# Kernel optimization log

Hardware: AMD Instinct MI355X
Metric: run time of the kernel (lower is better)

Reference implementation:

```python
import jax, jax.numpy as jnp
import numpy as np

B, S, D = 8, 512, 512
IN_S = IN_D = IN_E = 32
OUT_S = OUT_D = OUT_E = 32


def setup_inputs() -> dict:
    key = jax.random.key(0)
    ks = jax.random.split(key, 16)
    sc = 0.1
    return {
        "x_s": jax.random.normal(ks[0], (B, S, IN_S), jnp.float32),
        "x_d": jax.random.normal(ks[1], (B, D, IN_D), jnp.float32),
        "x_e": jax.random.normal(ks[2], (B, S, D, IN_E), jnp.float32),
        "W_ss": jax.random.normal(ks[3], (OUT_S, IN_S), jnp.float32) * sc,
        "b_ss": jnp.zeros((OUT_S,), jnp.float32),
        "W_se": jax.random.normal(ks[4], (OUT_S, IN_E), jnp.float32) * sc,
        "a_se_w": jax.random.normal(ks[5], (IN_E,), jnp.float32) * sc,
        "a_se_b": jnp.zeros((), jnp.float32),
        "W_dd": jax.random.normal(ks[6], (OUT_D, IN_D), jnp.float32) * sc,
        "b_dd": jnp.zeros((OUT_D,), jnp.float32),
        "W_de": jax.random.normal(ks[7], (OUT_D, IN_E), jnp.float32) * sc,
        "a_de_w": jax.random.normal(ks[8], (IN_E,), jnp.float32) * sc,
        "a_de_b": jnp.zeros((), jnp.float32),
        "W_ee": jax.random.normal(ks[9], (OUT_E, IN_E), jnp.float32) * sc,
        "b_ee": jnp.zeros((OUT_E,), jnp.float32),
        "W_es": jax.random.normal(ks[10], (OUT_E, IN_S), jnp.float32) * sc,
        "W_ed": jax.random.normal(ks[11], (OUT_E, IN_D), jnp.float32) * sc,
    }


def reference(x_s, x_d, x_e, W_ss, b_ss, W_se, a_se_w, a_se_b,
              W_dd, b_dd, W_de, a_de_w, a_de_b, W_ee, b_ee, W_es, W_ed):
    # Supply update: attention softmax over demand axis (dim=2)
    att_s = jax.nn.softmax(jnp.einsum('bsde,e->bsd', x_e, a_se_w) + a_se_b, axis=2)
    proj_se = jnp.einsum('bsde,oe->bsdo', x_e, W_se)
    h_s = jnp.einsum('bsi,oi->bso', x_s, W_ss) + b_ss \
        + jnp.einsum('bsdo,bsd->bso', proj_se, att_s)

    # Demand update: attention softmax over supply axis (dim=1)
    att_d = jax.nn.softmax(jnp.einsum('bsde,e->bsd', x_e, a_de_w) + a_de_b, axis=1)
    proj_de = jnp.einsum('bsde,oe->bsdo', x_e, W_de)
    h_d = jnp.einsum('bdi,oi->bdo', x_d, W_dd) + b_dd \
        + jnp.einsum('bsdo,bsd->bdo', proj_de, att_d)

    # Edge update: edge linear + broadcast node projections
    h_e = jnp.einsum('bsde,oe->bsdo', x_e, W_ee) + b_ee \
        + jnp.einsum('bsi,oi->bso', x_s, W_es)[:, :, None, :] \
        + jnp.einsum('bdi,oi->bdo', x_d, W_ed)[:, None, :, :]
    return (h_s, h_d, h_e)
```

## Files before the change

kernel.cpp:

```cpp
#include <hip/hip_runtime.h>
#include <cstddef>

#define B_ 8
#define S_ 512
#define D_ 512
#define TS 8
#define NST 64
#define DH 256

#define WS_BASES 0
#define WS_PES   131072
#define WS_BASED 262144
#define WS_PED   393216
#define WS_UD    524288
#define WS_ZD    (WS_UD + B_*NST*D_*32)
#define WS_US    (WS_ZD + B_*NST*D_)
#define WS_ZS    (WS_US + B_*S_*2*32)

#define HS_OFF 0
#define HD_OFF 131072
#define HE_OFF 262144

__global__ __launch_bounds__(256)
void k0_nodes(const float* __restrict__ x_s, const float* __restrict__ x_d,
              const float* __restrict__ W_ss, const float* __restrict__ b_ss,
              const float* __restrict__ W_dd, const float* __restrict__ b_dd,
              const float* __restrict__ W_es, const float* __restrict__ W_ed,
              float* __restrict__ ws)
{
  int g = blockIdx.x * 256 + threadIdx.x;
  int row = g >> 5, o = g & 31;
  bool sup = row < (B_ * S_);
  int r = sup ? row : row - B_ * S_;
  const float* x  = (sup ? x_s : x_d) + r * 32;
  const float* W1 = sup ? W_ss : W_dd;
  const float* W2 = sup ? W_es : W_ed;
  const float* bb = sup ? b_ss : b_dd;
  float xr[32];
#pragma unroll
  for (int k = 0; k < 8; k++)
    *(float4*)&xr[4*k] = *(const float4*)(x + 4*k);
  float acc1 = bb[o], acc2 = 0.f;
#pragma unroll
  for (int e = 0; e < 32; e++) {
    acc1 += xr[e] * W1[o*32 + e];
    acc2 += xr[e] * W2[o*32 + e];
  }
  int ob = sup ? WS_BASES : WS_BASED;
  int op = sup ? WS_PES  : WS_PED;
  ws[ob + r*32 + o] = acc1;
  ws[op + r*32 + o] = acc2;
}

__global__ __launch_bounds__(256, 3)
void k1_main(const float* __restrict__ x_e,
             const float* __restrict__ a_se_w, const float* __restrict__ a_se_b,
             const float* __restrict__ a_de_w, const float* __restrict__ a_de_b,
             const float* __restrict__ W_ee, const float* __restrict__ b_ee,
             float* __restrict__ ws,
             float* __restrict__ out)
{
  __shared__ float lds_ud[DH * 33];
  __shared__ float lds_hb[TS * 32];

  const int t = threadIdx.x;
  const int s_idx = t >> 5, d_off = t & 31;
  const int st = blockIdx.x, b = blockIdx.y, z = blockIdx.z;
  const int s = st * TS + s_idx;
  const int d0 = z * DH;

  for (int idx = t; idx < DH * 33; idx += 256) lds_ud[idx] = 0.f;
  lds_hb[t] = ws[WS_PES + (b*S_ + st*TS + (t>>5))*32 + (t&31)] + b_ee[t&31];
  __syncthreads();

  const float* xrow  = x_e + ((size_t)(b * S_ + s) * D_ + d0) * 32;
  float*       herow = out + HE_OFF + ((size_t)(b * S_ + s) * D_ + d0) * 32;
  const float* peD   = ws + WS_PED + ((size_t)b * D_ + d0) * 32;

  float us_acc[32];
#pragma unroll
  for (int e = 0; e < 32; e++) us_acc[e] = 0.f;
  float zs_acc = 0.f;
  const float asb = a_se_b[0], adb = a_de_b[0];

  float4 xb[8];
#pragma unroll
  for (int k = 0; k < 8; k++)
    xb[k] = *(const float4*)(xrow + d_off*32 + 4*k);

#pragma unroll 1
  for (int i = 0; i < 8; i++) {
    const int d = i*32 + d_off;
    float x[32];
#pragma unroll
    for (int k = 0; k < 8; k++) {
      x[4*k+0] = xb[k].x; x[4*k+1] = xb[k].y;
      x[4*k+2] = xb[k].z; x[4*k+3] = xb[k].w;
    }
    const int dn = (i < 7) ? d + 32 : d;
#pragma unroll
    for (int k = 0; k < 8; k++)
      xb[k] = *(const float4*)(xrow + dn*32 + 4*k);

    float ls = asb, ldt = adb;
#pragma unroll
    for (int e = 0; e < 32; e++) {
      ls  += x[e] * a_se_w[e];
      ldt += x[e] * a_de_w[e];
    }
    float es = __expf(ls), ed = __expf(ldt);
    zs_acc += es;
#pragma unroll
    for (int e = 0; e < 32; e++) us_acc[e] += es * x[e];

#pragma unroll
    for (int oq = 0; oq < 8; oq++) {
      float4 pdq = *(const float4*)(peD + d*32 + 4*oq);
      float4 hb  = *(const float4*)&lds_hb[s_idx*32 + 4*oq];
      float a0 = 0.f, a1 = 0.f, a2 = 0.f, a3 = 0.f;
#pragma unroll
      for (int e = 0; e < 32; e++) {
        a0 += x[e] * W_ee[(4*oq+0)*32 + e];
        a1 += x[e] * W_ee[(4*oq+1)*32 + e];
        a2 += x[e] * W_ee[(4*oq+2)*32 + e];
        a3 += x[e] * W_ee[(4*oq+3)*32 + e];
      }
      float4 r;
      r.x = a0 + hb.x + pdq.x;
      r.y = a1 + hb.y + pdq.y;
      r.z = a2 + hb.z + pdq.z;
      r.w = a3 + hb.w + pdq.w;
      *(float4*)(herow + d*32 + 4*oq) = r;
    }

#pragma unroll
    for (int e = 0; e < 32; e++)
      atomicAdd(&lds_ud[d*33 + e], ed * x[e]);
    atomicAdd(&lds_ud[d*33 + 32], ed);
  }
  __syncthreads();

  float* wud = ws + WS_UD + ((size_t)(b * NST + st) * D_ + d0) * 32;
  float* wzd = ws + WS_ZD + (b * NST + st) * D_ + d0;
#pragma unroll 1
  for (int sw = 0; sw < 8; sw++) {
    int r = sw * 32 + (t >> 3), g = t & 7;
    *(float4*)(wud + r*32 + g*4) = *(float4*)&lds_ud[r*33 + g*4];
  }
  wzd[t] = lds_ud[t*33 + 32];
  __syncthreads();

  float* red = lds_ud;
#pragma unroll
  for (int k = 0; k < 8; k++) {
    float4 v;
    v.x = us_acc[4*k+0]; v.y = us_acc[4*k+1];
    v.z = us_acc[4*k+2]; v.w = us_acc[4*k+3];
    *(float4*)&red[t*33 + 4*k] = v;
  }
  red[t*33 + 32] = zs_acc;
  __syncthreads();

  float sum = 0.f, zsum = 0.f;
#pragma unroll 1
  for (int dd = 0; dd < 32; dd++) {
    sum  += red[(s_idx*32 + dd)*33 + d_off];
    zsum += red[(s_idx*32 + dd)*33 + 32];
  }
  ws[WS_US + ((size_t)(b*S_ + s) * 2 + z) * 32 + d_off] = sum;
  if (d_off == 0) ws[WS_ZS + (b*S_ + s)*2 + z] = zsum;
}

__global__ __launch_bounds__(256)
void k2_hd(const float* __restrict__ W_de, const float* __restrict__ ws,
           float* __restrict__ out)
{
  __shared__ float lds_u[8 * 32];
  const int t = threadIdx.x;
  const int r = t >> 5, e = t & 31;
  const int b = blockIdx.x >> 6, dg = blockIdx.x & 63;
  const int d = dg * 8 + r;
  const float* wud = ws + WS_UD;
  const float* wzd = ws + WS_ZD;
  float sum = 0.f, z = 0.f;
#pragma unroll 4
  for (int st = 0; st < NST; st++) {
    sum += wud[((size_t)(b*NST + st) * D_ + d) * 32 + e];
    z   += wzd[(b*NST + st) * D_ + d];
  }
  lds_u[r*32 + e] = sum / z;
  __syncthreads();
  float acc = ws[WS_BASED + (b*D_ + d)*32 + e];
#pragma unroll
  for (int ee = 0; ee < 32; ee++)
    acc += W_de[e*32 + ee] * lds_u[r*32 + ee];
  out[HD_OFF + (b*D_ + d)*32 + e] = acc;
}

__global__ __launch_bounds__(256)
void k3_hs(const float* __restrict__ W_se, const float* __restrict__ ws,
           float* __restrict__ out)
{
  __shared__ float lds_u[8 * 32];
  const int t = threadIdx.x;
  const int r = t >> 5, e = t & 31;
  const int row = blockIdx.x * 8 + r;
  float U = ws[WS_US + ((size_t)row*2 + 0)*32 + e]
          + ws[WS_US + ((size_t)row*2 + 1)*32 + e];
  float Z = ws[WS_ZS + row*2 + 0] + ws[WS_ZS + row*2 + 1];
  lds_u[r*32 + e] = U / Z;
  __syncthreads();
  float acc = ws[WS_BASES + (size_t)row*32 + e];
#pragma unroll
  for (int ee = 0; ee < 32; ee++)
    acc += W_se[e*32 + ee] * lds_u[r*32 + ee];
  out[HS_OFF + (size_t)row*32 + e] = acc;
}

extern "C" void kernel_launch(void* const* d_in, const int* in_sizes, int n_in,
                              void* d_out, int out_size, void* d_ws, size_t ws_size,
                              hipStream_t stream)
{
  const float* x_s    = (const float*)d_in[0];
  const float* x_d    = (const float*)d_in[1];
  const float* x_e    = (const float*)d_in[2];
  const float* W_ss   = (const float*)d_in[3];
  const float* b_ss   = (const float*)d_in[4];
  const float* W_se   = (const float*)d_in[5];
  const float* a_se_w = (const float*)d_in[6];
  const float* a_se_b = (const float*)d_in[7];
  const float* W_dd   = (const float*)d_in[8];
  const float* b_dd   = (const float*)d_in[9];
  const float* W_de   = (const float*)d_in[10];
  const float* a_de_w = (const float*)d_in[11];
  const float* a_de_b = (const float*)d_in[12];
  const float* W_ee   = (const float*)d_in[13];
  const float* b_ee   = (const float*)d_in[14];
  const float* W_es   = (const float*)d_in[15];
  const float* W_ed   = (const float*)d_in[16];
  float* out = (float*)d_out;
  float* ws  = (float*)d_ws;

  hipLaunchKernelGGL(k0_nodes, dim3(1024), dim3(256), 0, stream,
                     x_s, x_d, W_ss, b_ss, W_dd, b_dd, W_es, W_ed, ws);
  hipLaunchKernelGGL(k1_main, dim3(NST, B_, 2), dim3(256), 0, stream,
                     x_e, a_se_w, a_se_b, a_de_w, a_de_b, W_ee, b_ee, ws, out);
  hipLaunchKernelGGL(k2_hd, dim3(512), dim3(256), 0, stream, W_de, ws, out);
  hipLaunchKernelGGL(k3_hs, dim3(512), dim3(256), 0, stream, W_se, ws, out);
}
```

Baseline: 947.5 us.

## Split demand axis into four chunks, halve LDS, merge tail kernels

Halves the demand chunk per block in the main edge kernel (DH 256→128, four z-slices), which doubles the grid and halves LDS use so more blocks fit per CU (launch bounds raised to 4). The per-supply reduction is done in two halves to fit the smaller LDS buffer, and the h_d and h_s finishing kernels are merged into one launch. More workgroups and partial sums to reduce, plus extra barriers, are the trade-off.

```diff
diff --git a/kernel.cpp b/kernel.cpp
--- a/kernel.cpp
+++ b/kernel.cpp
@@ -6,7 +6,8 @@
 #define D_ 512
 #define TS 8
 #define NST 64
-#define DH 256
+#define DH 128
+#define NZ 4
 
 #define WS_BASES 0
 #define WS_PES   131072
@@ -15,7 +16,7 @@
 #define WS_UD    524288
 #define WS_ZD    (WS_UD + B_*NST*D_*32)
 #define WS_US    (WS_ZD + B_*NST*D_)
-#define WS_ZS    (WS_US + B_*S_*2*32)
+#define WS_ZS    (WS_US + B_*S_*NZ*32)
 
 #define HS_OFF 0
 #define HD_OFF 131072
@@ -52,7 +53,7 @@
   ws[op + r*32 + o] = acc2;
 }
 
-__global__ __launch_bounds__(256, 3)
+__global__ __launch_bounds__(256, 4)
 void k1_main(const float* __restrict__ x_e,
              const float* __restrict__ a_se_w, const float* __restrict__ a_se_b,
              const float* __restrict__ a_de_w, const float* __restrict__ a_de_b,
@@ -89,7 +90,7 @@
     xb[k] = *(const float4*)(xrow + d_off*32 + 4*k);
 
 #pragma unroll 1
-  for (int i = 0; i < 8; i++) {
+  for (int i = 0; i < 4; i++) {
     const int d = i*32 + d_off;
     float x[32];
 #pragma unroll
@@ -97,7 +98,7 @@
       x[4*k+0] = xb[k].x; x[4*k+1] = xb[k].y;
       x[4*k+2] = xb[k].z; x[4*k+3] = xb[k].w;
     }
-    const int dn = (i < 7) ? d + 32 : d;
+    const int dn = (i < 3) ? d + 32 : d;
 #pragma unroll
     for (int k = 0; k < 8; k++)
       xb[k] = *(const float4*)(xrow + dn*32 + 4*k);
@@ -143,78 +144,103 @@
   float* wud = ws + WS_UD + ((size_t)(b * NST + st) * D_ + d0) * 32;
   float* wzd = ws + WS_ZD + (b * NST + st) * D_ + d0;
 #pragma unroll 1
-  for (int sw = 0; sw < 8; sw++) {
+  for (int sw = 0; sw < 4; sw++) {
     int r = sw * 32 + (t >> 3), g = t & 7;
     *(float4*)(wud + r*32 + g*4) = *(float4*)&lds_ud[r*33 + g*4];
   }
-  wzd[t] = lds_ud[t*33 + 32];
+  if (t < DH) wzd[t] = lds_ud[t*33 + 32];
   __syncthreads();
 
   float* red = lds_ud;
-#pragma unroll
-  for (int k = 0; k < 8; k++) {
-    float4 v;
-    v.x = us_acc[4*k+0]; v.y = us_acc[4*k+1];
-    v.z = us_acc[4*k+2]; v.w = us_acc[4*k+3];
-    *(float4*)&red[t*33 + 4*k] = v;
-  }
-  red[t*33 + 32] = zs_acc;
-  __syncthreads();
-
-  float sum = 0.f, zsum = 0.f;
-#pragma unroll 1
-  for (int dd = 0; dd < 32; dd++) {
-    sum  += red[(s_idx*32 + dd)*33 + d_off];
-    zsum += red[(s_idx*32 + dd)*33 + 32];
-  }
-  ws[WS_US + ((size_t)(b*S_ + s) * 2 + z) * 32 + d_off] = sum;
-  if (d_off == 0) ws[WS_ZS + (b*S_ + s)*2 + z] = zsum;
+  if (t < 128) {
+#pragma unroll
+    for (int k = 0; k < 8; k++) {
+      float4 v;
+      v.x = us_acc[4*k+0]; v.y = us_acc[4*k+1];
+      v.z = us_acc[4*k+2]; v.w = us_acc[4*k+3];
+      *(float4*)&red[t*33 + 4*k] = v;
+    }
+    red[t*33 + 32] = zs_acc;
+  }
+  __syncthreads();
+  if (t < 128) {
+    float sum = 0.f, zsum = 0.f;
+#pragma unroll 1
+    for (int dd = 0; dd < 32; dd++) {
+      sum  += red[(s_idx*32 + dd)*33 + d_off];
+      zsum += red[(s_idx*32 + dd)*33 + 32];
+    }
+    ws[WS_US + ((size_t)(b*S_ + s) * NZ + z) * 32 + d_off] = sum;
+    if (d_off == 0) ws[WS_ZS + (b*S_ + s)*NZ + z] = zsum;
+  }
+  __syncthreads();
+  if (t >= 128) {
+    const int tl = t - 128;
+#pragma unroll
+    for (int k = 0; k < 8; k++) {
+      float4 v;
+      v.x = us_acc[4*k+0]; v.y = us_acc[4*k+1];
+      v.z = us_acc[4*k+2]; v.w = us_acc[4*k+3];
+      *(float4*)&red[tl*33 + 4*k] = v;
+    }
+    red[tl*33 + 32] = zs_acc;
+  }
+  __syncthreads();
+  if (t >= 128) {
+    const int sl = s_idx - 4;
+    float sum = 0.f, zsum = 0.f;
+#pragma unroll 1
+    for (int dd = 0; dd < 32; dd++) {
+      sum  += red[(sl*32 + dd)*33 + d_off];
+      zsum += red[(sl*32 + dd)*33 + 32];
+    }
+    ws[WS_US + ((size_t)(b*S_ + s) * NZ + z) * 32 + d_off] = sum;
+    if (d_off == 0) ws[WS_ZS + (b*S_ + s)*NZ + z] = zsum;
+  }
 }
 
 __global__ __launch_bounds__(256)
-void k2_hd(const float* __restrict__ W_de, const float* __restrict__ ws,
-           float* __restrict__ out)
+void k2_tail(const float* __restrict__ W_de, const float* __restrict__ W_se,
+             const float* __restrict__ ws, float* __restrict__ out)
 {
   __shared__ float lds_u[8 * 32];
   const int t = threadIdx.x;
   const int r = t >> 5, e = t & 31;
-  const int b = blockIdx.x >> 6, dg = blockIdx.x & 63;
-  const int d = dg * 8 + r;
-  const float* wud = ws + WS_UD;
-  const float* wzd = ws + WS_ZD;
-  float sum = 0.f, z = 0.f;
+
+  if (blockIdx.x < 512) {
+    const int b = blockIdx.x >> 6, dg = blockIdx.x & 63;
+    const int d = dg * 8 + r;
+    const float* wud = ws + WS_UD;
+    const float* wzd = ws + WS_ZD;
+    float sum = 0.f, zv = 0.f;
 #pragma unroll 4
-  for (int st = 0; st < NST; st++) {
-    sum += wud[((size_t)(b*NST + st) * D_ + d) * 32 + e];
-    z   += wzd[(b*NST + st) * D_ + d];
-  }
-  lds_u[r*32 + e] = sum / z;
-  __syncthreads();
-  float acc = ws[WS_BASED + (b*D_ + d)*32 + e];
-#pragma unroll
-  for (int ee = 0; ee < 32; ee++)
-    acc += W_de[e*32 + ee] * lds_u[r*32 + ee];
-  out[HD_OFF + (b*D_ + d)*32 + e] = acc;
-}
-
-__global__ __launch_bounds__(256)
-void k3_hs(const float* __restrict__ W_se, const float* __restrict__ ws,
-           float* __restrict__ out)
-{
-  __shared__ float lds_u[8 * 32];
-  const int t = threadIdx.x;
-  const int r = t >> 5, e = t & 31;
-  const int row = blockIdx.x * 8 + r;
-  float U = ws[WS_US + ((size_t)row*2 + 0)*32 + e]
-          + ws[WS_US + ((size_t)row*2 + 1)*32 + e];
-  float Z = ws[WS_ZS + row*2 + 0] + ws[WS_ZS + row*2 + 1];
-  lds_u[r*32 + e] = U / Z;
-  __syncthreads();
-  float acc = ws[WS_BASES + (size_t)row*32 + e];
-#pragma unroll
-  for (int ee = 0; ee < 32; ee++)
-    acc += W_se[e*32 + ee] * lds_u[r*32 + ee];
-  out[HS_OFF + (size_t)row*32 + e] = acc;
+    for (int st = 0; st < NST; st++) {
+      sum += wud[((size_t)(b*NST + st) * D_ + d) * 32 + e];
+      zv  += wzd[(b*NST + st) * D_ + d];
+    }
+    lds_u[r*32 + e] = sum / zv;
+    __syncthreads();
+    float acc = ws[WS_BASED + (b*D_ + d)*32 + e];
+#pragma unroll
+    for (int ee = 0; ee < 32; ee++)
+      acc += W_de[e*32 + ee] * lds_u[r*32 + ee];
+    out[HD_OFF + (b*D_ + d)*32 + e] = acc;
+  } else {
+    const int row = (blockIdx.x - 512) * 8 + r;
+    float U = 0.f, Z = 0.f;
+#pragma unroll
+    for (int z = 0; z < NZ; z++) {
+      U += ws[WS_US + ((size_t)row*NZ + z)*32 + e];
+      Z += ws[WS_ZS + row*NZ + z];
+    }
+    lds_u[r*32 + e] = U / Z;
+    __syncthreads();
+    float acc = ws[WS_BASES + (size_t)row*32 + e];
+#pragma unroll
+    for (int ee = 0; ee < 32; ee++)
+      acc += W_se[e*32 + ee] * lds_u[r*32 + ee];
+    out[HS_OFF + (size_t)row*32 + e] = acc;
+  }
 }
 
 extern "C" void kernel_launch(void* const* d_in, const int* in_sizes, int n_in,
@@ -243,8 +269,7 @@
 
   hipLaunchKernelGGL(k0_nodes, dim3(1024), dim3(256), 0, stream,
                      x_s, x_d, W_ss, b_ss, W_dd, b_dd, W_es, W_ed, ws);
-  hipLaunchKernelGGL(k1_main, dim3(NST, B_, 2), dim3(256), 0, stream,
+  hipLaunchKernelGGL(k1_main, dim3(NST, B_, NZ), dim3(256), 0, stream,
                      x_e, a_se_w, a_se_b, a_de_w, a_de_b, W_ee, b_ee, ws, out);
-  hipLaunchKernelGGL(k2_hd, dim3(512), dim3(256), 0, stream, W_de, ws, out);
-  hipLaunchKernelGGL(k3_hs, dim3(512), dim3(256), 0, stream, W_se, ws, out);
-}
+  hipLaunchKernelGGL(k2_tail, dim3(1024), dim3(256), 0, stream, W_de, W_se, ws, out);
+}
```

After: 849.7 us. 10.3% less time.
